# Kernel tuning notes

Measured on AMD Instinct MI355X. Metric: run time of the kernel, lower is better.

## Reference

```python
import jax, jax.numpy as jnp
import numpy as np
from functools import partial

BLUR = 0.001      # entropic blur; for geomloss p=1 cost, eps = blur
SCALING = 0.9     # epsilon-scaling annealing ratio
# static iteration count covering log(blur/diameter)/log(scaling) for randn data
# (diameter ~ 9-16 => ~92 steps); extra steps run at eps=blur and only refine.
N_ITERS = 96


def _cost(x, y):
    """Euclidean cost ||x_i - y_j|| -> [B, N, M] (geomloss p=1 cost)."""
    x2 = jnp.sum(x * x, -1)[:, :, None]            # [B,N,1]
    y2 = jnp.sum(y * y, -1)[:, None, :]            # [B,1,M]
    xy = jnp.einsum('bnd,bmd->bnm', x, y)          # [B,N,M]
    sq = jnp.maximum(x2 + y2 - 2.0 * xy, 1e-12)
    return jnp.sqrt(sq)


def _softmin(eps, C, h_log):
    """-eps * logsumexp_j(h_log_j - C_ij/eps). C: [B,N,M], h_log: [B,M] -> [B,N]."""
    return -eps * jax.nn.logsumexp(h_log[:, None, :] - C / eps, axis=2)


def _sinkhorn_loss(x, y):
    B, N, _ = x.shape
    M = y.shape[1]
    a_log = jnp.full((B, N), -jnp.log(float(N)), dtype=x.dtype)  # uniform 1/N
    b_log = jnp.full((B, M), -jnp.log(float(M)), dtype=y.dtype)

    C_xy = _cost(x, y)                 # [B,N,M] (differentiable)
    C_yx = jnp.swapaxes(C_xy, 1, 2)    # [B,M,N]
    # sinkhorn loop runs on detached costs (geomloss detaches the loop)
    Cd_xy = jax.lax.stop_gradient(C_xy)
    Cd_yx = jax.lax.stop_gradient(C_yx)

    pts = jnp.concatenate([x, y], axis=1)
    diameter = jax.lax.stop_gradient(
        jnp.max(jnp.max(pts, axis=(0, 1)) - jnp.min(pts, axis=(0, 1))))
    ks = jnp.arange(N_ITERS, dtype=x.dtype)
    eps_list = jnp.maximum(diameter * SCALING ** ks, BLUR)  # annealing schedule

    f0 = _softmin(eps_list[0], Cd_xy, b_log)   # [B,N]
    g0 = _softmin(eps_list[0], Cd_yx, a_log)   # [B,M]

    def step(carry, eps):
        f, g = carry
        ft = _softmin(eps, Cd_xy, b_log + g / eps)
        gt = _softmin(eps, Cd_yx, a_log + f / eps)
        return ((f + ft) * 0.5, (g + gt) * 0.5), None

    (f, g), _ = jax.lax.scan(step, (f0, g0), eps_list)
    # final extrapolation step at eps=blur, differentiable w.r.t. x, y
    f_fin = _softmin(BLUR, C_xy, b_log + g / BLUR)   # g already detached
    g_fin = _softmin(BLUR, C_yx, a_log + f / BLUR)

    a = jnp.exp(a_log)
    b = jnp.exp(b_log)
    per_sample = jnp.sum(a * f_fin, axis=1) + jnp.sum(b * g_fin, axis=1)  # [B]
    return jnp.mean(per_sample)  # reduce='mean'


def setup_inputs() -> dict:
    key = jax.random.key(0)
    kx, ky = jax.random.split(key)
    x = jax.random.normal(kx, (2, 8192, 3), dtype=jnp.float32)
    y = jax.random.normal(ky, (2, 8192, 3), dtype=jnp.float32)
    return {"x": x, "y": y}


def reference(x, y):
    return _sinkhorn_loss(x, y)
```

## Files before the change

kernel.cpp:

```cpp
#include <hip/hip_runtime.h>
#include <math.h>

#define NPTS   8192
#define NB     2
#define NROWS  (NB*NPTS)
#define ROWS_PER_WAVE  8
#define WAVES_PER_BLOCK 4
#define ROWS_PER_BLOCK (ROWS_PER_WAVE*WAVES_PER_BLOCK)
#define BLURF  0.001f
#define LOG2E  1.4426950408889634f
#define LN2F   0.6931471805599453f
#define BLOGF  (-9.010913347279288f)

typedef float v2f __attribute__((ext_vector_type(2)));

#if __has_builtin(__builtin_amdgcn_sqrtf)
#define FAST_SQRT(x) __builtin_amdgcn_sqrtf(x)
#else
#define FAST_SQRT(x) sqrtf(x)
#endif
#if __has_builtin(__builtin_amdgcn_exp2f)
#define RAW_EXP2(x) __builtin_amdgcn_exp2f(x)
#else
#define RAW_EXP2(x) exp2f(x)
#endif
#if __has_builtin(__builtin_amdgcn_logf)
#define RAW_LOG2(x) __builtin_amdgcn_logf(x)
#else
#define RAW_LOG2(x) log2f(x)
#endif
#if __has_builtin(__builtin_elementwise_max)
#define PKMAX(a,b) __builtin_elementwise_max(a,b)
#else
static __device__ __forceinline__ v2f PKMAX(v2f a, v2f b){ v2f r; r.x=fmaxf(a.x,b.x); r.y=fmaxf(a.y,b.y); return r; }
#endif

#define WS_DIAM 0
#define WS_FA   16
#define WS_GA   (WS_FA + NROWS)
#define WS_XX   (WS_GA + NROWS)
#define WS_XY   (WS_XX + 3*NROWS)
#define WS_WXA  (WS_XY + 3*NROWS)
#define WS_WXB  (WS_WXA + NROWS)
#define WS_WYA  (WS_WXB + NROWS)
#define WS_WYB  (WS_WYA + NROWS)

__global__ __launch_bounds__(1024) void minmax_kernel(
    const float* __restrict__ x, const float* __restrict__ y,
    float* __restrict__ diam_out)
{
    int tid = threadIdx.x;
    float mx[3] = {-INFINITY, -INFINITY, -INFINITY};
    float mn[3] = { INFINITY,  INFINITY,  INFINITY};
    for (int p = tid; p < NROWS; p += 1024) {
        #pragma unroll
        for (int d = 0; d < 3; ++d) {
            float a = x[p*3+d], b = y[p*3+d];
            mx[d] = fmaxf(mx[d], fmaxf(a, b));
            mn[d] = fminf(mn[d], fminf(a, b));
        }
    }
    #pragma unroll
    for (int off = 32; off >= 1; off >>= 1) {
        #pragma unroll
        for (int d = 0; d < 3; ++d) {
            mx[d] = fmaxf(mx[d], __shfl_xor(mx[d], off));
            mn[d] = fminf(mn[d], __shfl_xor(mn[d], off));
        }
    }
    __shared__ float smx[16][3], smn[16][3];
    int wid = tid >> 6, lane = tid & 63;
    if (lane == 0) {
        #pragma unroll
        for (int d = 0; d < 3; ++d) { smx[wid][d] = mx[d]; smn[wid][d] = mn[d]; }
    }
    __syncthreads();
    if (tid == 0) {
        float dm = 0.0f;
        #pragma unroll
        for (int d = 0; d < 3; ++d) {
            float a = -INFINITY, b = INFINITY;
            for (int w = 0; w < 16; ++w) {
                a = fmaxf(a, smx[w][d]); b = fminf(b, smn[w][d]);
            }
            dm = fmaxf(dm, a - b);
        }
        diam_out[0] = dm;
    }
}

__global__ __launch_bounds__(256) void pack_pts_kernel(
    const float* __restrict__ x, const float* __restrict__ y,
    float* __restrict__ ws)
{
    int gid = blockIdx.x * 256 + threadIdx.x;
    int sel = gid >> 14;
    int idx = gid & (NROWS-1);
    const float* p = sel ? y : x;
    int off = sel ? WS_XY : WS_XX;
    ws[off + idx]           = p[idx*3+0];
    ws[off +   NROWS + idx] = p[idx*3+1];
    ws[off + 2*NROWS + idx] = p[idx*3+2];
    ws[(sel ? WS_WYA : WS_WXA) + idx] = BLOGF * LOG2E;
}

__global__ __launch_bounds__(256, 4) void softmin_kernel(
    const float* __restrict__ x, const float* __restrict__ y,
    float* __restrict__ ws, int cur,
    float scale_k, float scale_next, int do_avg)
{
    const int dir = blockIdx.z;
    const float* rows = dir ? y : x;

    const float diam      = ws[WS_DIAM];
    const float eps       = fmaxf(diam * scale_k, BLURF);
    const float nie2      = -LOG2E / eps;
    const float eps_next  = fmaxf(diam * scale_next, BLURF);
    const float ien_log2e = LOG2E / eps_next;

    const int tid = threadIdx.x, lane = tid & 63, wid = tid >> 6;
    const int i0  = blockIdx.x * ROWS_PER_BLOCK;
    const int b   = i0 >> 13;
    const int rowbase = i0 + wid * ROWS_PER_WAVE;

    const int cbase = dir ? WS_XX : WS_XY;
    const v2f* CX = ((const v2f*)(ws + cbase          )) + b*(NPTS/2);
    const v2f* CY = ((const v2f*)(ws + cbase +   NROWS)) + b*(NPTS/2);
    const v2f* CZ = ((const v2f*)(ws + cbase + 2*NROWS)) + b*(NPTS/2);
    const int wcur_off = dir ? (cur ? WS_WXB : WS_WXA) : (cur ? WS_WYB : WS_WYA);
    const int wnxt_off = dir ? (cur ? WS_WYA : WS_WYB) : (cur ? WS_WXA : WS_WXB);
    const v2f* CW = ((const v2f*)(ws + wcur_off)) + b*(NPTS/2);
    float* Wnxt = ws + wnxt_off;
    float* outf = ws + (dir ? WS_GA : WS_FA);

    float px[8], py[8], pz[8];
    #pragma unroll
    for (int r = 0; r < 8; ++r) {
        int o = (rowbase + r) * 3;
        px[r] = rows[o]; py[r] = rows[o+1]; pz[r] = rows[o+2];
    }

    v2f m2[8], s2[8];
    #pragma unroll
    for (int r = 0; r < 8; ++r) { m2[r] = (v2f){-INFINITY,-INFINITY}; s2[r] = (v2f){0.0f,0.0f}; }

    const v2f nie2v = {nie2, nie2};

    for (int c0 = 0; c0 < NPTS/2; c0 += 256) {
        v2f Xc[4], Yc[4], Zc[4], Wc[4];
        #pragma unroll
        for (int k = 0; k < 4; ++k) {
            int idx = c0 + k*64 + lane;
            Xc[k] = CX[idx]; Yc[k] = CY[idx]; Zc[k] = CZ[idx]; Wc[k] = CW[idx];
        }
        #pragma unroll
        for (int r = 0; r < 8; ++r) {
            const v2f prx = {px[r], px[r]}, pry = {py[r], py[r]}, prz = {pz[r], pz[r]};
            v2f w2[4];
            #pragma unroll
            for (int k = 0; k < 4; ++k) {
                v2f dx = Xc[k] - prx, dy = Yc[k] - pry, dz = Zc[k] - prz;
                v2f sq = dx*dx + dy*dy + dz*dz;
                v2f c2; c2.x = FAST_SQRT(sq.x); c2.y = FAST_SQRT(sq.y);
                w2[k] = c2 * nie2v + Wc[k];
            }
            v2f gm = PKMAX(PKMAX(w2[0], w2[1]), PKMAX(w2[2], w2[3]));
            v2f mu = PKMAX(m2[r], gm);
            v2f dm = m2[r] - mu;
            v2f e0 = w2[0] - mu, e1 = w2[1] - mu, e2 = w2[2] - mu, e3 = w2[3] - mu;
            float ex = (RAW_EXP2(e0.x) + RAW_EXP2(e1.x)) + (RAW_EXP2(e2.x) + RAW_EXP2(e3.x));
            float ey = (RAW_EXP2(e0.y) + RAW_EXP2(e1.y)) + (RAW_EXP2(e2.y) + RAW_EXP2(e3.y));
            s2[r].x = fmaf(s2[r].x, RAW_EXP2(dm.x), ex);
            s2[r].y = fmaf(s2[r].y, RAW_EXP2(dm.y), ey);
            m2[r] = mu;
        }
    }

    #pragma unroll
    for (int r = 0; r < 8; ++r) {
        float mm = fmaxf(m2[r].x, m2[r].y);
        float ss = s2[r].x * RAW_EXP2(m2[r].x - mm) + s2[r].y * RAW_EXP2(m2[r].y - mm);
        #pragma unroll
        for (int off = 32; off >= 1; off >>= 1) {
            float mo = __shfl_xor(mm, off);
            float so = __shfl_xor(ss, off);
            float mu = fmaxf(mm, mo);
            ss = fmaf(ss, RAW_EXP2(mm-mu), so * RAW_EXP2(mo-mu));
            mm = mu;
        }
        if (lane == 0) {
            float res = -eps * LN2F * (mm + RAW_LOG2(ss));
            int oidx = rowbase + r;
            if (do_avg) res = 0.5f * (outf[oidx] + res);
            outf[oidx] = res;
            Wnxt[oidx] = fmaf(res, ien_log2e, BLOGF * LOG2E);
        }
    }
}

__global__ __launch_bounds__(1024) void reduce_kernel(
    const float* __restrict__ ws, float* __restrict__ out)
{
    const float* f = ws + WS_FA;
    const float* g = ws + WS_GA;
    int tid = threadIdx.x;
    float acc = 0.0f;
    for (int i = tid; i < NROWS; i += 1024) acc += f[i] + g[i];
    #pragma unroll
    for (int off = 32; off >= 1; off >>= 1) acc += __shfl_xor(acc, off);
    __shared__ float sw[16];
    int wid = tid >> 6, lane = tid & 63;
    if (lane == 0) sw[wid] = acc;
    __syncthreads();
    if (tid == 0) {
        float t = 0.0f;
        for (int w = 0; w < 16; ++w) t += sw[w];
        out[0] = t * (1.0f / (float)NROWS);
    }
}

extern "C" void kernel_launch(void* const* d_in, const int* in_sizes, int n_in,
                              void* d_out, int out_size, void* d_ws, size_t ws_size,
                              hipStream_t stream)
{
    const float* x = (const float*)d_in[0];
    const float* y = (const float*)d_in[1];
    float* out = (float*)d_out;
    float* ws  = (float*)d_ws;

    minmax_kernel<<<1, 1024, 0, stream>>>(x, y, ws + WS_DIAM);
    pack_pts_kernel<<<(NROWS*2)/256, 256, 0, stream>>>(x, y, ws);

    dim3 sgrid(NROWS/ROWS_PER_BLOCK, 1, 2);
    int cur = 0;

    softmin_kernel<<<sgrid, 256, 0, stream>>>(x, y, ws, cur, 1.0f, 1.0f, 0);
    cur ^= 1;

    double sk = 1.0;
    for (int k = 0; k < 96; ++k) {
        float sn = (k < 95) ? (float)(sk * 0.9) : 0.0f;
        softmin_kernel<<<sgrid, 256, 0, stream>>>(x, y, ws, cur, (float)sk, sn, 1);
        cur ^= 1;
        sk *= 0.9;
    }

    softmin_kernel<<<sgrid, 256, 0, stream>>>(x, y, ws, cur, 0.0f, 0.0f, 0);

    reduce_kernel<<<1, 1024, 0, stream>>>(ws, out);
}
```

Measured before the change: 8.942 ms.

## Defer online-softmax rescaling with wave-uniform threshold and halve rows per wave

The online logsumexp now updates its running max only when some lane's new block max exceeds the stored max by more than a threshold of 8 in log2 units, checked with a wave-wide any-vote. This removes the per-step rescale exp2 calls in the common case. Rows per wave drop from 8 to 4, which doubles the block count and halves reuse of each loaded column tile across rows. The deferral lets partial exponentials reach up to 2^8 per term before rescaling, relying on fp32 range, and adds a divergent branch per row step.

```diff
diff --git a/kernel.cpp b/kernel.cpp
--- a/kernel.cpp
+++ b/kernel.cpp
@@ -4,13 +4,14 @@
 #define NPTS   8192
 #define NB     2
 #define NROWS  (NB*NPTS)
-#define ROWS_PER_WAVE  8
+#define ROWS_PER_WAVE  4
 #define WAVES_PER_BLOCK 4
 #define ROWS_PER_BLOCK (ROWS_PER_WAVE*WAVES_PER_BLOCK)
 #define BLURF  0.001f
 #define LOG2E  1.4426950408889634f
 #define LN2F   0.6931471805599453f
 #define BLOGF  (-9.010913347279288f)
+#define DEFER_THR 8.0f
 
 typedef float v2f __attribute__((ext_vector_type(2)));
 
@@ -133,16 +134,18 @@
     float* Wnxt = ws + wnxt_off;
     float* outf = ws + (dir ? WS_GA : WS_FA);
 
-    float px[8], py[8], pz[8];
-    #pragma unroll
-    for (int r = 0; r < 8; ++r) {
+    float px[ROWS_PER_WAVE], py[ROWS_PER_WAVE], pz[ROWS_PER_WAVE];
+    #pragma unroll
+    for (int r = 0; r < ROWS_PER_WAVE; ++r) {
         int o = (rowbase + r) * 3;
         px[r] = rows[o]; py[r] = rows[o+1]; pz[r] = rows[o+2];
     }
 
-    v2f m2[8], s2[8];
-    #pragma unroll
-    for (int r = 0; r < 8; ++r) { m2[r] = (v2f){-INFINITY,-INFINITY}; s2[r] = (v2f){0.0f,0.0f}; }
+    v2f m2[ROWS_PER_WAVE], s2[ROWS_PER_WAVE];
+    #pragma unroll
+    for (int r = 0; r < ROWS_PER_WAVE; ++r) {
+        m2[r] = (v2f){-INFINITY,-INFINITY}; s2[r] = (v2f){0.0f,0.0f};
+    }
 
     const v2f nie2v = {nie2, nie2};
 
@@ -154,7 +157,7 @@
             Xc[k] = CX[idx]; Yc[k] = CY[idx]; Zc[k] = CZ[idx]; Wc[k] = CW[idx];
         }
         #pragma unroll
-        for (int r = 0; r < 8; ++r) {
+        for (int r = 0; r < ROWS_PER_WAVE; ++r) {
             const v2f prx = {px[r], px[r]}, pry = {py[r], py[r]}, prz = {pz[r], pz[r]};
             v2f w2[4];
             #pragma unroll
@@ -165,19 +168,26 @@
                 w2[k] = c2 * nie2v + Wc[k];
             }
             v2f gm = PKMAX(PKMAX(w2[0], w2[1]), PKMAX(w2[2], w2[3]));
-            v2f mu = PKMAX(m2[r], gm);
-            v2f dm = m2[r] - mu;
-            v2f e0 = w2[0] - mu, e1 = w2[1] - mu, e2 = w2[2] - mu, e3 = w2[3] - mu;
-            float ex = (RAW_EXP2(e0.x) + RAW_EXP2(e1.x)) + (RAW_EXP2(e2.x) + RAW_EXP2(e3.x));
-            float ey = (RAW_EXP2(e0.y) + RAW_EXP2(e1.y)) + (RAW_EXP2(e2.y) + RAW_EXP2(e3.y));
-            s2[r].x = fmaf(s2[r].x, RAW_EXP2(dm.x), ex);
-            s2[r].y = fmaf(s2[r].y, RAW_EXP2(dm.y), ey);
-            m2[r] = mu;
-        }
-    }
-
-    #pragma unroll
-    for (int r = 0; r < 8; ++r) {
+            bool need = (gm.x > m2[r].x + DEFER_THR) | (gm.y > m2[r].y + DEFER_THR);
+            if (__any(need)) {
+                v2f mu = PKMAX(m2[r], gm);
+                v2f dm = m2[r] - mu;
+                v2f sc; sc.x = RAW_EXP2(dm.x); sc.y = RAW_EXP2(dm.y);
+                s2[r] = s2[r] * sc;
+                m2[r] = mu;
+            }
+            v2f e0 = w2[0] - m2[r], e1 = w2[1] - m2[r], e2 = w2[2] - m2[r], e3 = w2[3] - m2[r];
+            v2f v0, v1, v2, v3;
+            v0.x = RAW_EXP2(e0.x); v0.y = RAW_EXP2(e0.y);
+            v1.x = RAW_EXP2(e1.x); v1.y = RAW_EXP2(e1.y);
+            v2.x = RAW_EXP2(e2.x); v2.y = RAW_EXP2(e2.y);
+            v3.x = RAW_EXP2(e3.x); v3.y = RAW_EXP2(e3.y);
+            s2[r] = s2[r] + ((v0 + v1) + (v2 + v3));
+        }
+    }
+
+    #pragma unroll
+    for (int r = 0; r < ROWS_PER_WAVE; ++r) {
         float mm = fmaxf(m2[r].x, m2[r].y);
         float ss = s2[r].x * RAW_EXP2(m2[r].x - mm) + s2[r].y * RAW_EXP2(m2[r].y - mm);
         #pragma unroll
```

Result: no change. 8.932 ms (-0.1%).
